# Kernel tuning notes

Measured on AMD Instinct MI355X. Metric: run time of the kernel, lower is better.

Reference implementation:

```python
import jax, jax.numpy as jnp
import numpy as np

N_NODES = 100000
N_EDGES = 1250000
HIDDEN = 64


def setup_inputs() -> dict:
    key = jax.random.key(0)
    ks = jax.random.split(key, 8)
    x = jax.random.normal(ks[0], (N_NODES, HIDDEN), dtype=jnp.float32)
    edge_index = jax.random.randint(ks[1], (2, N_EDGES), 0, N_NODES, dtype=jnp.int64)
    s = 1.0 / np.sqrt(HIDDEN)
    # PyG SAGEConv params: lin_l (neighbor path, with bias), lin_r (root path, no bias)
    W1l = jax.random.uniform(ks[2], (HIDDEN, HIDDEN), jnp.float32, -s, s)
    b1l = jnp.zeros((HIDDEN,), jnp.float32)
    W1r = jax.random.uniform(ks[3], (HIDDEN, HIDDEN), jnp.float32, -s, s)
    W2l = jax.random.uniform(ks[4], (HIDDEN, HIDDEN), jnp.float32, -s, s)
    b2l = jnp.zeros((HIDDEN,), jnp.float32)
    W2r = jax.random.uniform(ks[5], (HIDDEN, HIDDEN), jnp.float32, -s, s)
    return {"x": x, "edge_index": edge_index, "W1l": W1l, "b1l": b1l,
            "W1r": W1r, "W2l": W2l, "b2l": b2l, "W2r": W2r}


def _sage_conv(x, src, dst, Wl, bl, Wr, num_nodes):
    # mean-aggregate neighbor (source) features at target nodes
    agg = jax.ops.segment_sum(x[src], dst, num_segments=num_nodes)  # [N, H]
    cnt = jax.ops.segment_sum(jnp.ones((src.shape[0],), x.dtype), dst,
                              num_segments=num_nodes)               # [N]
    mean = agg / jnp.maximum(cnt, 1.0)[:, None]
    # out = lin_l(mean_neighbors) + lin_r(x_root)
    return mean @ Wl + bl + x @ Wr


def reference(x, edge_index, W1l, b1l, W1r, W2l, b2l, W2r):
    src, dst = edge_index[0], edge_index[1]
    n = x.shape[0]
    h = jax.nn.relu(_sage_conv(x, src, dst, W1l, b1l, W1r, n))
    return _sage_conv(h, src, dst, W2l, b2l, W2r, n)
```

## Files before the change

### kernel.cpp

```cpp
#include <hip/hip_runtime.h>
#include <hip/hip_bf16.h>

#define HIDDEN 64
#define TN 64
#define MPAD 68
#define SRCM 0x01FFFFFF

__global__ __launch_bounds__(256) void k_hist(
    const int* __restrict__ ei, int* __restrict__ deg, int nEdges)
{
    for (int e = blockIdx.x * blockDim.x + threadIdx.x; e < nEdges;
         e += gridDim.x * blockDim.x) {
        atomicAdd(&deg[ei[nEdges + e]], 1);
    }
}

__global__ __launch_bounds__(256) void k_scan1(
    const int* __restrict__ deg, int* __restrict__ rowPtr,
    int* __restrict__ blockSum, int n)
{
    __shared__ int tmp[256];
    const int t = threadIdx.x;
    const int i = blockIdx.x * 256 + t;
    const int v = (i < n) ? deg[i] : 0;
    tmp[t] = v;
    __syncthreads();
#pragma unroll
    for (int off = 1; off < 256; off <<= 1) {
        const int u = (t >= off) ? tmp[t - off] : 0;
        __syncthreads();
        tmp[t] += u;
        __syncthreads();
    }
    if (i < n) rowPtr[i] = tmp[t] - v;
    if (t == 255) blockSum[blockIdx.x] = tmp[255];
}

__global__ __launch_bounds__(512) void k_scan2(
    int* __restrict__ blockSum, int* __restrict__ rowPtr, int nb, int n)
{
    __shared__ int tmp[512];
    const int t = threadIdx.x;
    const int v = (t < nb) ? blockSum[t] : 0;
    tmp[t] = v;
    __syncthreads();
#pragma unroll
    for (int off = 1; off < 512; off <<= 1) {
        const int u = (t >= off) ? tmp[t - off] : 0;
        __syncthreads();
        tmp[t] += u;
        __syncthreads();
    }
    if (t < nb) blockSum[t] = tmp[t] - v;
    if (t == nb - 1) rowPtr[n] = tmp[t];
}

__global__ __launch_bounds__(256) void k_scan3(
    int* __restrict__ rowPtr, int* __restrict__ cursor,
    const int* __restrict__ blockSum, int n)
{
    const int i = blockIdx.x * 256 + threadIdx.x;
    if (i < n) {
        const int v = rowPtr[i] + blockSum[blockIdx.x];
        rowPtr[i] = v;
        cursor[i] = v;
    }
}

__global__ __launch_bounds__(256) void k_fill(
    const int* __restrict__ ei, int* __restrict__ cursor,
    int* __restrict__ csrSrc, int nEdges)
{
    for (int e = blockIdx.x * blockDim.x + threadIdx.x; e < nEdges;
         e += gridDim.x * blockDim.x) {
        const int dst = ei[nEdges + e];
        const int pos = atomicAdd(&cursor[dst], 1);
        csrSrc[pos] = ei[e] | ((dst & 63) << 25);
    }
}

template <bool RELU>
__global__ __launch_bounds__(512, 6) void k_fused(
    const float* __restrict__ xin,
    const int* __restrict__ rowPtr,
    const int* __restrict__ csrSrc,
    const float* __restrict__ Wl,
    const float* __restrict__ bl,
    const float* __restrict__ Wr,
    float* __restrict__ outp,
    int nNodes)
{
    __shared__ __align__(16) float sM[TN][MPAD];
    __shared__ __align__(16) float sB[2 * HIDDEN][HIDDEN];
    __shared__ float sInv[TN];

    const int tid  = threadIdx.x;
    const int w    = tid >> 6;
    const int lane = tid & 63;
    const int base = blockIdx.x * TN;

    for (int i = tid; i < HIDDEN * HIDDEN; i += 512) {
        sB[i >> 6][i & 63]          = Wl[i];
        sB[(i >> 6) + HIDDEN][i & 63] = Wr[i];
    }
    for (int idx = tid; idx < TN * 16; idx += 512)
        *(float4*)&sM[idx >> 4][(idx & 15) * 4] = make_float4(0.f, 0.f, 0.f, 0.f);
    if (tid < TN) {
        const int g = base + tid;
        float iv = 1.f;
        if (g < nNodes) {
            const int d = rowPtr[g + 1] - rowPtr[g];
            if (d > 0) iv = 1.f / (float)d;
        }
        sInv[tid] = iv;
    }
    __syncthreads();

    {
        const int eBeg = rowPtr[base];
        const int eEnd = rowPtr[min(base + TN, nNodes)];
        int e = eBeg + w * 8;
#pragma unroll 1
        for (; e + 8 <= eEnd; e += 64) {
            int   pk[8];
            float v[8];
#pragma unroll
            for (int k = 0; k < 8; ++k) pk[k] = csrSrc[e + k];
#pragma unroll
            for (int k = 0; k < 8; ++k)
                v[k] = xin[(pk[k] & SRCM) * HIDDEN + lane];
#pragma unroll
            for (int k = 0; k < 8; ++k)
                atomicAdd(&sM[pk[k] >> 25][lane], v[k]);
        }
        if (e < eEnd) {
#pragma unroll 1
            for (; e < eEnd; ++e) {
                const int p = csrSrc[e];
                atomicAdd(&sM[p >> 25][lane], xin[(p & SRCM) * HIDDEN + lane]);
            }
        }
    }
    __syncthreads();

    for (int idx = tid; idx < TN * 16; idx += 512) {
        const int row = idx >> 4, c4 = (idx & 15) * 4;
        float4 v = *(const float4*)&sM[row][c4];
        const float iv = sInv[row];
        v.x *= iv; v.y *= iv; v.z *= iv; v.w *= iv;
        *(float4*)&sM[row][c4] = v;
    }
    __syncthreads();

    const int team = tid >> 8;
    const int tt   = tid & 255;
    const int tr   = tt >> 4;
    const int tc   = tt & 15;
    float acc[4][4];

    if (team == 0) {
#pragma unroll
        for (int r = 0; r < 4; ++r)
#pragma unroll
            for (int j = 0; j < 4; ++j) acc[r][j] = 0.f;
#pragma unroll
        for (int k4 = 0; k4 < 16; ++k4) {
            float4 A4[4], B4[4];
#pragma unroll
            for (int r = 0; r < 4; ++r)
                A4[r] = *(const float4*)&sM[tr * 4 + r][k4 * 4];
#pragma unroll
            for (int kk = 0; kk < 4; ++kk)
                B4[kk] = *(const float4*)&sB[k4 * 4 + kk][tc * 4];
#pragma unroll
            for (int r = 0; r < 4; ++r) {
                acc[r][0] = fmaf(A4[r].x, B4[0].x, acc[r][0]);
                acc[r][1] = fmaf(A4[r].x, B4[0].y, acc[r][1]);
                acc[r][2] = fmaf(A4[r].x, B4[0].z, acc[r][2]);
                acc[r][3] = fmaf(A4[r].x, B4[0].w, acc[r][3]);
                acc[r][0] = fmaf(A4[r].y, B4[1].x, acc[r][0]);
                acc[r][1] = fmaf(A4[r].y, B4[1].y, acc[r][1]);
                acc[r][2] = fmaf(A4[r].y, B4[1].z, acc[r][2]);
                acc[r][3] = fmaf(A4[r].y, B4[1].w, acc[r][3]);
                acc[r][0] = fmaf(A4[r].z, B4[2].x, acc[r][0]);
                acc[r][1] = fmaf(A4[r].z, B4[2].y, acc[r][1]);
                acc[r][2] = fmaf(A4[r].z, B4[2].z, acc[r][2]);
                acc[r][3] = fmaf(A4[r].z, B4[2].w, acc[r][3]);
                acc[r][0] = fmaf(A4[r].w, B4[3].x, acc[r][0]);
                acc[r][1] = fmaf(A4[r].w, B4[3].y, acc[r][1]);
                acc[r][2] = fmaf(A4[r].w, B4[3].z, acc[r][2]);
                acc[r][3] = fmaf(A4[r].w, B4[3].w, acc[r][3]);
            }
        }
    } else {
        const float* xr[4];
#pragma unroll
        for (int r = 0; r < 4; ++r) {
            int g = base + tr * 4 + r;
            g = (g < nNodes) ? g : 0;
            xr[r] = xin + g * HIDDEN;
        }
#pragma unroll
        for (int r = 0; r < 4; ++r)
#pragma unroll
            for (int j = 0; j < 4; ++j) acc[r][j] = bl[tc * 4 + j];
#pragma unroll
        for (int k4 = 0; k4 < 16; ++k4) {
            float4 A4[4], B4[4];
#pragma unroll
            for (int r = 0; r < 4; ++r)
                A4[r] = *(const float4*)(xr[r] + k4 * 4);
#pragma unroll
            for (int kk = 0; kk < 4; ++kk)
                B4[kk] = *(const float4*)&sB[HIDDEN + k4 * 4 + kk][tc * 4];
#pragma unroll
            for (int r = 0; r < 4; ++r) {
                acc[r][0] = fmaf(A4[r].x, B4[0].x, acc[r][0]);
                acc[r][1] = fmaf(A4[r].x, B4[0].y, acc[r][1]);
                acc[r][2] = fmaf(A4[r].x, B4[0].z, acc[r][2]);
                acc[r][3] = fmaf(A4[r].x, B4[0].w, acc[r][3]);
                acc[r][0] = fmaf(A4[r].y, B4[1].x, acc[r][0]);
                acc[r][1] = fmaf(A4[r].y, B4[1].y, acc[r][1]);
                acc[r][2] = fmaf(A4[r].y, B4[1].z, acc[r][2]);
                acc[r][3] = fmaf(A4[r].y, B4[1].w, acc[r][3]);
                acc[r][0] = fmaf(A4[r].z, B4[2].x, acc[r][0]);
                acc[r][1] = fmaf(A4[r].z, B4[2].y, acc[r][1]);
                acc[r][2] = fmaf(A4[r].z, B4[2].z, acc[r][2]);
                acc[r][3] = fmaf(A4[r].z, B4[2].w, acc[r][3]);
                acc[r][0] = fmaf(A4[r].w, B4[3].x, acc[r][0]);
                acc[r][1] = fmaf(A4[r].w, B4[3].y, acc[r][1]);
                acc[r][2] = fmaf(A4[r].w, B4[3].z, acc[r][2]);
                acc[r][3] = fmaf(A4[r].w, B4[3].w, acc[r][3]);
            }
        }
    }
    __syncthreads();

    if (team == 1) {
#pragma unroll
        for (int r = 0; r < 4; ++r) {
            float4 st;
            st.x = acc[r][0]; st.y = acc[r][1];
            st.z = acc[r][2]; st.w = acc[r][3];
            *(float4*)&sM[tr * 4 + r][tc * 4] = st;
        }
    }
    __syncthreads();
    if (team == 0) {
#pragma unroll
        for (int r = 0; r < 4; ++r) {
            const int g = base + tr * 4 + r;
            if (g < nNodes) {
                const float4 c4 = *(const float4*)&sM[tr * 4 + r][tc * 4];
                float4 o;
                o.x = acc[r][0] + c4.x; o.y = acc[r][1] + c4.y;
                o.z = acc[r][2] + c4.z; o.w = acc[r][3] + c4.w;
                if (RELU) {
                    o.x = fmaxf(o.x, 0.f); o.y = fmaxf(o.y, 0.f);
                    o.z = fmaxf(o.z, 0.f); o.w = fmaxf(o.w, 0.f);
                }
                *(float4*)&outp[g * HIDDEN + tc * 4] = o;
            }
        }
    }
}

extern "C" void kernel_launch(void* const* d_in, const int* in_sizes, int n_in,
                              void* d_out, int out_size, void* d_ws, size_t ws_size,
                              hipStream_t stream)
{
    const float* x   = (const float*)d_in[0];
    const int*   ei  = (const int*)d_in[1];
    const float* W1l = (const float*)d_in[2];
    const float* b1l = (const float*)d_in[3];
    const float* W1r = (const float*)d_in[4];
    const float* W2l = (const float*)d_in[5];
    const float* b2l = (const float*)d_in[6];
    const float* W2r = (const float*)d_in[7];
    float* out = (float*)d_out;

    const int nNodes = in_sizes[0] / HIDDEN;
    const int nEdges = in_sizes[1] / 2;

    float* h        = (float*)d_ws;
    int*   deg      = (int*)(h + (size_t)nNodes * HIDDEN);
    int*   rowPtr   = deg + (nNodes + 1);
    int*   cursor   = rowPtr + (nNodes + 1);
    int*   csrSrc   = cursor + nNodes;
    int*   blockSum = csrSrc + nEdges;

    const int nTiles  = (nNodes + TN - 1) / TN;
    const int nChunks = (nNodes + 255) / 256;

    hipMemsetAsync(deg, 0, (size_t)(nNodes + 1) * sizeof(int), stream);
    k_hist<<<2048, 256, 0, stream>>>(ei, deg, nEdges);
    k_scan1<<<nChunks, 256, 0, stream>>>(deg, rowPtr, blockSum, nNodes);
    k_scan2<<<1, 512, 0, stream>>>(blockSum, rowPtr, nChunks, nNodes);
    k_scan3<<<nChunks, 256, 0, stream>>>(rowPtr, cursor, blockSum, nNodes);
    k_fill<<<2048, 256, 0, stream>>>(ei, cursor, csrSrc, nEdges);

    k_fused<true><<<nTiles, 512, 0, stream>>>(x, rowPtr, csrSrc, W1l, b1l, W1r,
                                              h, nNodes);
    k_fused<false><<<nTiles, 512, 0, stream>>>(h, rowPtr, csrSrc, W2l, b2l, W2r,
                                               out, nNodes);
}
```

Before: 1.207 ms.

## Gather neighbor features in bf16 and store hidden layer as bf16

```diff
diff --git a/kernel.cpp b/kernel.cpp
--- a/kernel.cpp
+++ b/kernel.cpp
@@ -5,6 +5,15 @@
 #define TN 64
 #define MPAD 68
 #define SRCM 0x01FFFFFF
+
+static __device__ __forceinline__ unsigned short f2bf(float f) {
+    unsigned int u = __float_as_uint(f);
+    u += 0x7FFF + ((u >> 16) & 1);
+    return (unsigned short)(u >> 16);
+}
+static __device__ __forceinline__ float bf2f(unsigned short s) {
+    return __uint_as_float((unsigned int)s << 16);
+}
 
 __global__ __launch_bounds__(256) void k_hist(
     const int* __restrict__ ei, int* __restrict__ deg, int nEdges)
@@ -79,15 +88,33 @@
     }
 }
 
-template <bool RELU>
+__global__ __launch_bounds__(256) void k_tobf16(
+    const float* __restrict__ src, unsigned short* __restrict__ dst, int n8)
+{
+    for (int i = blockIdx.x * 256 + threadIdx.x; i < n8; i += gridDim.x * 256) {
+        const float4 a = ((const float4*)src)[2 * i];
+        const float4 b = ((const float4*)src)[2 * i + 1];
+        uint4 o;
+        o.x = (unsigned)f2bf(a.x) | ((unsigned)f2bf(a.y) << 16);
+        o.y = (unsigned)f2bf(a.z) | ((unsigned)f2bf(a.w) << 16);
+        o.z = (unsigned)f2bf(b.x) | ((unsigned)f2bf(b.y) << 16);
+        o.w = (unsigned)f2bf(b.z) | ((unsigned)f2bf(b.w) << 16);
+        ((uint4*)dst)[i] = o;
+    }
+}
+
+template <bool RELU, bool OUT_BF16, bool ROOT_BF16>
 __global__ __launch_bounds__(512, 6) void k_fused(
-    const float* __restrict__ xin,
+    const unsigned short* __restrict__ gtab,
+    const float* __restrict__ rootf,
+    const unsigned short* __restrict__ rootb,
     const int* __restrict__ rowPtr,
     const int* __restrict__ csrSrc,
     const float* __restrict__ Wl,
     const float* __restrict__ bl,
     const float* __restrict__ Wr,
     float* __restrict__ outp,
+    unsigned short* __restrict__ goutb,
     int nNodes)
 {
     __shared__ __align__(16) float sM[TN][MPAD];
@@ -100,7 +127,7 @@
     const int base = blockIdx.x * TN;
 
     for (int i = tid; i < HIDDEN * HIDDEN; i += 512) {
-        sB[i >> 6][i & 63]          = Wl[i];
+        sB[i >> 6][i & 63]            = Wl[i];
         sB[(i >> 6) + HIDDEN][i & 63] = Wr[i];
     }
     for (int idx = tid; idx < TN * 16; idx += 512)
@@ -119,25 +146,31 @@
     {
         const int eBeg = rowPtr[base];
         const int eEnd = rowPtr[min(base + TN, nNodes)];
-        int e = eBeg + w * 8;
+        const int half = lane >> 5;
+        const int f2   = (lane & 31) * 2;
+        int e = eBeg + w * 16;
 #pragma unroll 1
-        for (; e + 8 <= eEnd; e += 64) {
-            int   pk[8];
-            float v[8];
-#pragma unroll
-            for (int k = 0; k < 8; ++k) pk[k] = csrSrc[e + k];
-#pragma unroll
-            for (int k = 0; k < 8; ++k)
-                v[k] = xin[(pk[k] & SRCM) * HIDDEN + lane];
-#pragma unroll
-            for (int k = 0; k < 8; ++k)
-                atomicAdd(&sM[pk[k] >> 25][lane], v[k]);
+        for (; e + 16 <= eEnd; e += 128) {
+            int pk[8];
+            unsigned int val[8];
+#pragma unroll
+            for (int p = 0; p < 8; ++p)
+                pk[p] = csrSrc[e + 2 * p + half];
+#pragma unroll
+            for (int p = 0; p < 8; ++p)
+                val[p] = *(const unsigned int*)&gtab[(pk[p] & SRCM) * HIDDEN + f2];
+#pragma unroll
+            for (int p = 0; p < 8; ++p) {
+                atomicAdd(&sM[pk[p] >> 25][f2],     __uint_as_float(val[p] << 16));
+                atomicAdd(&sM[pk[p] >> 25][f2 + 1], __uint_as_float(val[p] & 0xFFFF0000u));
+            }
         }
         if (e < eEnd) {
 #pragma unroll 1
             for (; e < eEnd; ++e) {
-                const int p = csrSrc[e];
-                atomicAdd(&sM[p >> 25][lane], xin[(p & SRCM) * HIDDEN + lane]);
+                const int pk = csrSrc[e];
+                const unsigned short u = gtab[(pk & SRCM) * HIDDEN + lane];
+                atomicAdd(&sM[pk >> 25][lane], bf2f(u));
             }
         }
     }
@@ -193,23 +226,29 @@
             }
         }
     } else {
-        const float* xr[4];
+#pragma unroll
+        for (int r = 0; r < 4; ++r)
+#pragma unroll
+            for (int j = 0; j < 4; ++j) acc[r][j] = bl[tc * 4 + j];
+        int gr[4];
 #pragma unroll
         for (int r = 0; r < 4; ++r) {
             int g = base + tr * 4 + r;
-            g = (g < nNodes) ? g : 0;
-            xr[r] = xin + g * HIDDEN;
-        }
-#pragma unroll
-        for (int r = 0; r < 4; ++r)
-#pragma unroll
-            for (int j = 0; j < 4; ++j) acc[r][j] = bl[tc * 4 + j];
+            gr[r] = (g < nNodes) ? g : 0;
+        }
 #pragma unroll
         for (int k4 = 0; k4 < 16; ++k4) {
             float4 A4[4], B4[4];
 #pragma unroll
-            for (int r = 0; r < 4; ++r)
-                A4[r] = *(const float4*)(xr[r] + k4 * 4);
+            for (int r = 0; r < 4; ++r) {
+                if (ROOT_BF16) {
+                    const ushort4 u4 = *(const ushort4*)&rootb[gr[r] * HIDDEN + k4 * 4];
+                    A4[r].x = bf2f(u4.x); A4[r].y = bf2f(u4.y);
+                    A4[r].z = bf2f(u4.z); A4[r].w = bf2f(u4.w);
+                } else {
+                    A4[r] = *(const float4*)&rootf[gr[r] * HIDDEN + k4 * 4];
+                }
+            }
 #pragma unroll
             for (int kk = 0; kk < 4; ++kk)
                 B4[kk] = *(const float4*)&sB[HIDDEN + k4 * 4 + kk][tc * 4];
@@ -259,7 +298,14 @@
                     o.x = fmaxf(o.x, 0.f); o.y = fmaxf(o.y, 0.f);
                     o.z = fmaxf(o.z, 0.f); o.w = fmaxf(o.w, 0.f);
                 }
-                *(float4*)&outp[g * HIDDEN + tc * 4] = o;
+                if (OUT_BF16) {
+                    ushort4 q;
+                    q.x = f2bf(o.x); q.y = f2bf(o.y);
+                    q.z = f2bf(o.z); q.w = f2bf(o.w);
+                    *(ushort4*)&goutb[g * HIDDEN + tc * 4] = q;
+                } else {
+                    *(float4*)&outp[g * HIDDEN + tc * 4] = o;
+                }
             }
         }
     }
@@ -282,15 +328,17 @@
     const int nNodes = in_sizes[0] / HIDDEN;
     const int nEdges = in_sizes[1] / 2;
 
-    float* h        = (float*)d_ws;
-    int*   deg      = (int*)(h + (size_t)nNodes * HIDDEN);
-    int*   rowPtr   = deg + (nNodes + 1);
-    int*   cursor   = rowPtr + (nNodes + 1);
-    int*   csrSrc   = cursor + nNodes;
-    int*   blockSum = csrSrc + nEdges;
+    unsigned short* cb2      = (unsigned short*)d_ws;
+    int*            deg      = (int*)(cb2 + (size_t)nNodes * HIDDEN);
+    int*            rowPtr   = deg + (nNodes + 1);
+    int*            cursor   = rowPtr + (nNodes + 1);
+    int*            csrSrc   = cursor + nNodes;
+    int*            blockSum = csrSrc + nEdges;
+    unsigned short* cb1      = (unsigned short*)d_out;
 
     const int nTiles  = (nNodes + TN - 1) / TN;
     const int nChunks = (nNodes + 255) / 256;
+    const int nFeat8  = nNodes * HIDDEN / 8;
 
     hipMemsetAsync(deg, 0, (size_t)(nNodes + 1) * sizeof(int), stream);
     k_hist<<<2048, 256, 0, stream>>>(ei, deg, nEdges);
@@ -299,8 +347,10 @@
     k_scan3<<<nChunks, 256, 0, stream>>>(rowPtr, cursor, blockSum, nNodes);
     k_fill<<<2048, 256, 0, stream>>>(ei, cursor, csrSrc, nEdges);
 
-    k_fused<true><<<nTiles, 512, 0, stream>>>(x, rowPtr, csrSrc, W1l, b1l, W1r,
-                                              h, nNodes);
-    k_fused<false><<<nTiles, 512, 0, stream>>>(h, rowPtr, csrSrc, W2l, b2l, W2r,
-                                               out, nNodes);
-}
+    k_tobf16<<<2048, 256, 0, stream>>>(x, cb1, nFeat8);
+    k_fused<true, true, false><<<nTiles, 512, 0, stream>>>(
+        cb1, x, nullptr, rowPtr, csrSrc, W1l, b1l, W1r, nullptr, cb2, nNodes);
+
+    k_fused<false, false, true><<<nTiles, 512, 0, stream>>>(
+        cb2, nullptr, cb2, rowPtr, csrSrc, W2l, b2l, W2r, out, nullptr, nNodes);
+}
```

Result: no change. 1.205 ms (-0.2%).
